# Performance work log

Measured on AMD Instinct MI355X. Metric: run time of the kernel, lower is better.

Reference implementation:

```python
import jax, jax.numpy as jnp
import numpy as np

B, N, D = 4, 4096, 256

def setup_inputs() -> dict:
    key = jax.random.key(0)
    k1, = jax.random.split(key, 1)
    x = jax.random.normal(k1, (B, N, D), dtype=jnp.float32)
    attn_mask = jnp.ones((B, 1, N), dtype=jnp.int32)
    pad_mask = jnp.ones((B, 1, N), dtype=jnp.int32)
    return {"x": x, "attn_mask": attn_mask, "pad_mask": pad_mask, "dim_": D}

def reference(x, attn_mask, pad_mask, dim_):
    # adj is None -> scores = x @ x^T / sqrt(d)
    scale = jnp.sqrt(jnp.asarray(x.shape[-1], x.dtype))
    scores = jnp.einsum('bnd,bmd->bnm', x, x) / scale  # [B, N, N]
    # NOTE: original calls non-in-place masked_fill and discards the result,
    # so pad_mask / attn_mask have no effect on the output (faithful).
    prob = jax.nn.softmax(scores, axis=-1)
    # dropout is identity in inference mode
    return jnp.einsum('bnm,bmd->bnd', prob, x)
```

## Files before the change

kernel.cpp:

```cpp
#include <hip/hip_runtime.h>

typedef __attribute__((ext_vector_type(8))) short short8;
typedef __attribute__((ext_vector_type(4))) float f32x4;
typedef __attribute__((ext_vector_type(4))) unsigned int u32x4;

#define NTOK 4096
#define DIM  256
#define P_STRIDE 72
#define TILE_ELEMS 32768

__device__ __forceinline__ unsigned pack2bf(float a, float b) {
  unsigned ua = __builtin_bit_cast(unsigned, a) + 0x8000u;
  unsigned ub = __builtin_bit_cast(unsigned, b) + 0x8000u;
  return __builtin_amdgcn_perm(ub, ua, 0x07060302u);
}

__global__ __launch_bounds__(256, 4)
void prep_kernel(const float* __restrict__ X, unsigned short* __restrict__ Img) {
  __shared__ __align__(16) unsigned short rowbf[8 * 256];
  const int b    = blockIdx.x & 3;
  const int sub  = blockIdx.x >> 2;
  const int t    = sub >> 3;
  const int part = sub & 7;
  const int tid  = threadIdx.x;
  const float* src = X + ((size_t)b * NTOK + t * 64 + part * 8) * DIM;
  unsigned short* dst = Img + ((size_t)(b * 64 + t)) * TILE_ELEMS;
  {
    const int r = tid >> 5;
    const int c = tid & 31;
    const float* s = src + r * DIM + c * 8;
    f32x4 f0 = *(const f32x4*)s;
    f32x4 f1 = *(const f32x4*)(s + 4);
    union { unsigned u[4]; u32x4 v; } p;
    p.u[0] = pack2bf(f0[0], f0[1]);
    p.u[1] = pack2bf(f0[2], f0[3]);
    p.u[2] = pack2bf(f1[0], f1[1]);
    p.u[3] = pack2bf(f1[2], f1[3]);
    const int gr = part * 8 + r;
    *(u32x4*)(dst + gr * 256 + ((c ^ (gr & 7)) << 3)) = p.v;
    *(u32x4*)(&rowbf[r * 256 + c * 8]) = p.v;
  }
  __syncthreads();
  {
    const int d = tid;
    union { unsigned short s[8]; u32x4 v; } p;
    #pragma unroll
    for (int i = 0; i < 8; ++i) p.s[i] = rowbf[i * 256 + d];
    *(u32x4*)(dst + 16384 + part * 2048 + d * 8) = p.v;
  }
}

__device__ __forceinline__ void pv_step(const unsigned short* __restrict__ pr,
                                        const unsigned short* __restrict__ kt,
                                        f32x4 (&o)[2][4],
                                        int qh, int role, int quad, int ln) {
  #pragma unroll
  for (int ks = 0; ks < 2; ++ks) {
    const int pos = (ks * 4 + quad) ^ ((ln >> 3) << 1);
    short8 ap[2], bv[4];
    #pragma unroll
    for (int s = 0; s < 2; ++s) {
      const int r = qh * 32 + s * 16 + ln;
      ap[s] = *(const short8*)(&pr[r * P_STRIDE + (pos << 3)]);
    }
    const unsigned short* kb = kt + (ks * 4 + quad) * 2048 + (role * 64 + ln) * 8;
    #pragma unroll
    for (int dt = 0; dt < 4; ++dt) bv[dt] = *(const short8*)(kb + dt * 128);
    #pragma unroll
    for (int s = 0; s < 2; ++s)
      #pragma unroll
      for (int dt = 0; dt < 4; ++dt)
        o[s][dt] = __builtin_amdgcn_mfma_f32_16x16x32_bf16(ap[s], bv[dt], o[s][dt], 0, 0, 0);
  }
}

__global__ __launch_bounds__(512, 1)
void fa_kernel(const unsigned short* __restrict__ Img, float* __restrict__ Out) {
  __shared__ __align__(16) unsigned short ksb[2][16384];
  __shared__ __align__(16) unsigned short ktb[2][16384];
  __shared__ __align__(16) unsigned short pb[2][64 * P_STRIDE];
  __shared__ float lbuf[64][4];

  const int tid  = threadIdx.x;
  const int b    = blockIdx.x & 3;
  const int qblk = blockIdx.x >> 2;
  const int wave = tid >> 6;
  const int lane = tid & 63;
  const int ln   = lane & 15;
  const int quad = lane >> 4;
  const int swz  = ln & 7;
  const int qh   = wave & 1;
  const int role = wave >> 1;

  const unsigned short* imgb  = Img + (size_t)b * 64 * TILE_ELEMS;
  const char*           imgbc = (const char*)imgb;

  short8 aQ[2][8];
  #pragma unroll
  for (int s = 0; s < 2; ++s) {
    const unsigned short* qrow =
        imgb + (size_t)qblk * TILE_ELEMS + (qh * 32 + s * 16 + ln) * 256;
    #pragma unroll
    for (int ds = 0; ds < 8; ++ds)
      aQ[s][ds] = *(const short8*)(qrow + (((ds * 4 + quad) ^ swz) << 3));
  }

  f32x4 o[2][4];
  #pragma unroll
  for (int s = 0; s < 2; ++s)
    #pragma unroll
    for (int dt = 0; dt < 4; ++dt) o[s][dt] = (f32x4)(0.0f);
  float lrow[2][4] = {{0.f,0.f,0.f,0.f},{0.f,0.f,0.f,0.f}};

  const float c2 = 0.0901684400f;

  const int pwPos = ((role * 2 + (ln >> 3)) ^ ((quad >> 1) << 1)) << 3;
  const int pwCol = ln & 7;

  const bool dmaKs = wave < 4;
  const int  dmaQ  = wave & 3;
  const char* gK = imgbc + (size_t)dmaQ * 8192 + (size_t)lane * 16;

  if (dmaKs) {
    #pragma unroll
    for (int i = 0; i < 8; ++i)
      __builtin_amdgcn_global_load_lds(
          (const __attribute__((address_space(1))) unsigned*)(gK + i * 1024),
          (__attribute__((address_space(3))) unsigned*)(&ksb[0][dmaQ * 4096 + i * 512]),
          16, 0, 0);
  }

  for (int t = 0; t < 64; ++t) {
    __syncthreads();
    const int buf = t & 1;

    if (dmaKs) {
      if (t < 63) {
        const char* g = gK + (size_t)(t + 1) * 65536;
        unsigned short* l = &ksb[buf ^ 1][dmaQ * 4096];
        #pragma unroll
        for (int i = 0; i < 8; ++i)
          __builtin_amdgcn_global_load_lds(
              (const __attribute__((address_space(1))) unsigned*)(g + i * 1024),
              (__attribute__((address_space(3))) unsigned*)(l + i * 512),
              16, 0, 0);
      }
    } else {
      const char* g = gK + (size_t)t * 65536 + 32768;
      unsigned short* l = &ktb[buf][dmaQ * 4096];
      #pragma unroll
      for (int i = 0; i < 8; ++i)
        __builtin_amdgcn_global_load_lds(
            (const __attribute__((address_space(1))) unsigned*)(g + i * 1024),
            (__attribute__((address_space(3))) unsigned*)(l + i * 512),
            16, 0, 0);
    }

    f32x4 sf0 = (f32x4)(0.0f), sf1 = (f32x4)(0.0f);
    {
      const unsigned short* krow = &ksb[buf][(role * 16 + ln) * 256];
      #pragma unroll
      for (int ds = 0; ds < 8; ++ds) {
        short8 bk = *(const short8*)(krow + (((ds * 4 + quad) ^ swz) << 3));
        sf0 = __builtin_amdgcn_mfma_f32_16x16x32_bf16(aQ[0][ds], bk, sf0, 0, 0, 0);
        sf1 = __builtin_amdgcn_mfma_f32_16x16x32_bf16(aQ[1][ds], bk, sf1, 0, 0, 0);
      }
    }

    unsigned pd0[4], pd1[4];
    #pragma unroll
    for (int j = 0; j < 4; ++j) {
      float p0 = __builtin_amdgcn_exp2f(sf0[j] * c2);
      float p1 = __builtin_amdgcn_exp2f(sf1[j] * c2);
      lrow[0][j] += p0;
      lrow[1][j] += p1;
      unsigned q0 = __builtin_bit_cast(unsigned, p0);
      unsigned q1 = __builtin_bit_cast(unsigned, p1);
      unsigned n0 = (unsigned)__builtin_amdgcn_mov_dpp((int)q0, 0xB1, 0xF, 0xF, true);
      unsigned n1 = (unsigned)__builtin_amdgcn_mov_dpp((int)q1, 0xB1, 0xF, 0xF, true);
      pd0[j] = pack2bf(__builtin_bit_cast(float, q0), __builtin_bit_cast(float, n0));
      pd1[j] = pack2bf(__builtin_bit_cast(float, q1), __builtin_bit_cast(float, n1));
    }

    if (t > 0)
      pv_step(pb[buf ^ 1], ktb[buf ^ 1], o, qh, role, quad, ln);

    if ((ln & 1) == 0) {
      unsigned short* pw = pb[buf];
      #pragma unroll
      for (int j = 0; j < 4; ++j) {
        const int r0 = qh * 32 + quad * 4 + j;
        *(unsigned*)(&pw[r0 * P_STRIDE + pwPos + pwCol]) = pd0[j];
        *(unsigned*)(&pw[(r0 + 16) * P_STRIDE + pwPos + pwCol]) = pd1[j];
      }
    }
  }

  __syncthreads();
  pv_step(pb[1], ktb[1], o, qh, role, quad, ln);

  #pragma unroll
  for (int off = 1; off < 16; off <<= 1)
    #pragma unroll
    for (int s = 0; s < 2; ++s)
      #pragma unroll
      for (int j = 0; j < 4; ++j)
        lrow[s][j] += __shfl_xor(lrow[s][j], off, 64);
  if (ln == 0) {
    #pragma unroll
    for (int s = 0; s < 2; ++s)
      #pragma unroll
      for (int j = 0; j < 4; ++j)
        lbuf[qh * 32 + s * 16 + quad * 4 + j][role] = lrow[s][j];
  }
  __syncthreads();

  #pragma unroll
  for (int s = 0; s < 2; ++s) {
    float* outp = Out + (size_t)(b * NTOK + qblk * 64 + qh * 32 + s * 16) * DIM + role * 64;
    #pragma unroll
    for (int j = 0; j < 4; ++j) {
      const int row = s * 16 + quad * 4 + j;
      f32x4 lv = *(const f32x4*)lbuf[qh * 32 + row];
      const float rl = 1.0f / (lv[0] + lv[1] + lv[2] + lv[3]);
      #pragma unroll
      for (int dt = 0; dt < 4; ++dt)
        outp[(size_t)(quad * 4 + j) * DIM + dt * 16 + ln] = o[s][dt][j] * rl;
    }
  }
}

extern "C" void kernel_launch(void* const* d_in, const int* in_sizes, int n_in,
                              void* d_out, int out_size, void* d_ws, size_t ws_size,
                              hipStream_t stream) {
  const float* X = (const float*)d_in[0];
  float* Out = (float*)d_out;
  unsigned short* Img = (unsigned short*)d_ws;
  (void)in_sizes; (void)n_in; (void)out_size; (void)ws_size;
  hipLaunchKernelGGL(prep_kernel, dim3(2048), dim3(256), 0, stream, X, Img);
  hipLaunchKernelGGL(fa_kernel, dim3(256), dim3(512), 0, stream, Img, Out);
}
```

Measured before the change: 165.7 us.

## Load transposed K tiles directly into registers instead of staging through LDS

The transposed K (V) operand for the PV matmul is now loaded from global memory straight into registers, one iteration ahead, using ping-pong register sets with a loop unrolled by two. The ktb LDS buffers are removed, and all 8 waves now share the score-K DMA into LDS with half the per-wave load count. The aim is to cut LDS traffic and footprint and spread the DMA work across every wave. In exchange, each wave now holds more registers and every wave reads its V fragments from global memory, where before they were loaded once into shared memory. That adds global and L2 traffic and may expose load latency.

```diff
diff --git a/kernel.cpp b/kernel.cpp
--- a/kernel.cpp
+++ b/kernel.cpp
@@ -50,34 +50,28 @@
   }
 }
 
-__device__ __forceinline__ void pv_step(const unsigned short* __restrict__ pr,
-                                        const unsigned short* __restrict__ kt,
-                                        f32x4 (&o)[2][4],
-                                        int qh, int role, int quad, int ln) {
+__device__ __forceinline__ void pv_reg(const unsigned short* __restrict__ pr,
+                                       const short8 (&bv)[2][4],
+                                       f32x4 (&o)[2][4],
+                                       int qh, int quad, int ln) {
   #pragma unroll
   for (int ks = 0; ks < 2; ++ks) {
     const int pos = (ks * 4 + quad) ^ ((ln >> 3) << 1);
-    short8 ap[2], bv[4];
-    #pragma unroll
-    for (int s = 0; s < 2; ++s) {
-      const int r = qh * 32 + s * 16 + ln;
-      ap[s] = *(const short8*)(&pr[r * P_STRIDE + (pos << 3)]);
-    }
-    const unsigned short* kb = kt + (ks * 4 + quad) * 2048 + (role * 64 + ln) * 8;
-    #pragma unroll
-    for (int dt = 0; dt < 4; ++dt) bv[dt] = *(const short8*)(kb + dt * 128);
+    short8 ap[2];
+    #pragma unroll
+    for (int s = 0; s < 2; ++s)
+      ap[s] = *(const short8*)(&pr[(qh * 32 + s * 16 + ln) * P_STRIDE + (pos << 3)]);
     #pragma unroll
     for (int s = 0; s < 2; ++s)
       #pragma unroll
       for (int dt = 0; dt < 4; ++dt)
-        o[s][dt] = __builtin_amdgcn_mfma_f32_16x16x32_bf16(ap[s], bv[dt], o[s][dt], 0, 0, 0);
+        o[s][dt] = __builtin_amdgcn_mfma_f32_16x16x32_bf16(ap[s], bv[ks][dt], o[s][dt], 0, 0, 0);
   }
 }
 
 __global__ __launch_bounds__(512, 1)
 void fa_kernel(const unsigned short* __restrict__ Img, float* __restrict__ Out) {
   __shared__ __align__(16) unsigned short ksb[2][16384];
-  __shared__ __align__(16) unsigned short ktb[2][16384];
   __shared__ __align__(16) unsigned short pb[2][64 * P_STRIDE];
   __shared__ float lbuf[64][4];
 
@@ -117,43 +111,42 @@
   const int pwPos = ((role * 2 + (ln >> 3)) ^ ((quad >> 1) << 1)) << 3;
   const int pwCol = ln & 7;
 
-  const bool dmaKs = wave < 4;
-  const int  dmaQ  = wave & 3;
-  const char* gK = imgbc + (size_t)dmaQ * 8192 + (size_t)lane * 16;
-
-  if (dmaKs) {
-    #pragma unroll
-    for (int i = 0; i < 8; ++i)
-      __builtin_amdgcn_global_load_lds(
-          (const __attribute__((address_space(1))) unsigned*)(gK + i * 1024),
-          (__attribute__((address_space(3))) unsigned*)(&ksb[0][dmaQ * 4096 + i * 512]),
-          16, 0, 0);
-  }
-
-  for (int t = 0; t < 64; ++t) {
+  const char* gK = imgbc + (size_t)wave * 4096 + (size_t)lane * 16;
+  #pragma unroll
+  for (int i = 0; i < 4; ++i)
+    __builtin_amdgcn_global_load_lds(
+        (const __attribute__((address_space(1))) unsigned*)(gK + i * 1024),
+        (__attribute__((address_space(3))) unsigned*)(&ksb[0][wave * 2048 + i * 512]),
+        16, 0, 0);
+
+  const unsigned short* ktg = imgb + 16384 + (size_t)quad * 2048 + (role * 64 + ln) * 8;
+
+  short8 bvE[2][4];
+  short8 bvO[2][4];
+
+  auto iter = [&](int t, short8 (&bvLd)[2][4], short8 (&bvUs)[2][4],
+                  bool doPV) __attribute__((always_inline)) {
     __syncthreads();
     const int buf = t & 1;
 
-    if (dmaKs) {
-      if (t < 63) {
-        const char* g = gK + (size_t)(t + 1) * 65536;
-        unsigned short* l = &ksb[buf ^ 1][dmaQ * 4096];
-        #pragma unroll
-        for (int i = 0; i < 8; ++i)
-          __builtin_amdgcn_global_load_lds(
-              (const __attribute__((address_space(1))) unsigned*)(g + i * 1024),
-              (__attribute__((address_space(3))) unsigned*)(l + i * 512),
-              16, 0, 0);
-      }
-    } else {
-      const char* g = gK + (size_t)t * 65536 + 32768;
-      unsigned short* l = &ktb[buf][dmaQ * 4096];
-      #pragma unroll
-      for (int i = 0; i < 8; ++i)
+    if (t < 63) {
+      const char* g = gK + (size_t)(t + 1) * 65536;
+      unsigned short* l = &ksb[buf ^ 1][wave * 2048];
+      #pragma unroll
+      for (int i = 0; i < 4; ++i)
         __builtin_amdgcn_global_load_lds(
             (const __attribute__((address_space(1))) unsigned*)(g + i * 1024),
             (__attribute__((address_space(3))) unsigned*)(l + i * 512),
             16, 0, 0);
+    }
+
+    {
+      const unsigned short* kt = ktg + (size_t)t * TILE_ELEMS;
+      #pragma unroll
+      for (int ks = 0; ks < 2; ++ks)
+        #pragma unroll
+        for (int dt = 0; dt < 4; ++dt)
+          bvLd[ks][dt] = *(const short8*)(kt + ks * 8192 + dt * 128);
     }
 
     f32x4 sf0 = (f32x4)(0.0f), sf1 = (f32x4)(0.0f);
@@ -182,8 +175,8 @@
       pd1[j] = pack2bf(__builtin_bit_cast(float, q1), __builtin_bit_cast(float, n1));
     }
 
-    if (t > 0)
-      pv_step(pb[buf ^ 1], ktb[buf ^ 1], o, qh, role, quad, ln);
+    if (doPV)
+      pv_reg(pb[buf ^ 1], bvUs, o, qh, quad, ln);
 
     if ((ln & 1) == 0) {
       unsigned short* pw = pb[buf];
@@ -194,10 +187,18 @@
         *(unsigned*)(&pw[(r0 + 16) * P_STRIDE + pwPos + pwCol]) = pd1[j];
       }
     }
-  }
+  };
+
+  iter(0, bvE, bvO, false);
+  #pragma unroll 1
+  for (int tt = 1; tt < 63; tt += 2) {
+    iter(tt, bvO, bvE, true);
+    iter(tt + 1, bvE, bvO, true);
+  }
+  iter(63, bvO, bvE, true);
 
   __syncthreads();
-  pv_step(pb[1], ktb[1], o, qh, role, quad, ln);
+  pv_reg(pb[1], bvO, o, qh, quad, ln);
 
   #pragma unroll
   for (int off = 1; off < 16; off <<= 1)
```

New measurement: 166.3 us. No clear change (+0.4%).

## Split each tile iteration into four barrier-synchronized phases interleaving loads and MFMA

Applied to the files above, without the earlier changes.

Restructures the main loop into four phases (two QK^T halves, two PV halves). Each phase issues LDS reads and splits the global-to-LDS DMA into halves, then crosses a raw s_barrier before running its MFMA cluster at raised wave priority. This ping-pong style schedule is meant to keep loads and matrix work overlapping across waves and to spread memory traffic evenly. It adds four barriers per iteration instead of one, so synchronization overhead and the risk of hazards from the manual waitcnt placement both increase.

```diff
diff --git a/kernel.cpp b/kernel.cpp
--- a/kernel.cpp
+++ b/kernel.cpp
@@ -50,30 +50,6 @@
   }
 }
 
-__device__ __forceinline__ void pv_step(const unsigned short* __restrict__ pr,
-                                        const unsigned short* __restrict__ kt,
-                                        f32x4 (&o)[2][4],
-                                        int qh, int role, int quad, int ln) {
-  #pragma unroll
-  for (int ks = 0; ks < 2; ++ks) {
-    const int pos = (ks * 4 + quad) ^ ((ln >> 3) << 1);
-    short8 ap[2], bv[4];
-    #pragma unroll
-    for (int s = 0; s < 2; ++s) {
-      const int r = qh * 32 + s * 16 + ln;
-      ap[s] = *(const short8*)(&pr[r * P_STRIDE + (pos << 3)]);
-    }
-    const unsigned short* kb = kt + (ks * 4 + quad) * 2048 + (role * 64 + ln) * 8;
-    #pragma unroll
-    for (int dt = 0; dt < 4; ++dt) bv[dt] = *(const short8*)(kb + dt * 128);
-    #pragma unroll
-    for (int s = 0; s < 2; ++s)
-      #pragma unroll
-      for (int dt = 0; dt < 4; ++dt)
-        o[s][dt] = __builtin_amdgcn_mfma_f32_16x16x32_bf16(ap[s], bv[dt], o[s][dt], 0, 0, 0);
-  }
-}
-
 __global__ __launch_bounds__(512, 1)
 void fa_kernel(const unsigned short* __restrict__ Img, float* __restrict__ Out) {
   __shared__ __align__(16) unsigned short ksb[2][16384];
@@ -129,75 +105,188 @@
           (__attribute__((address_space(3))) unsigned*)(&ksb[0][dmaQ * 4096 + i * 512]),
           16, 0, 0);
   }
-
+  __syncthreads();
+
+  #pragma unroll 1
   for (int t = 0; t < 64; ++t) {
-    __syncthreads();
     const int buf = t & 1;
-
-    if (dmaKs) {
-      if (t < 63) {
-        const char* g = gK + (size_t)(t + 1) * 65536;
-        unsigned short* l = &ksb[buf ^ 1][dmaQ * 4096];
-        #pragma unroll
-        for (int i = 0; i < 8; ++i)
+    const unsigned short* krow = &ksb[buf][(role * 16 + ln) * 256];
+    const unsigned short* prd  = pb[buf ^ 1];
+    const unsigned short* ktp  = ktb[buf ^ 1];
+    const char* gNext = gK + (size_t)(t + 1) * 65536;
+    unsigned short* lNext = &ksb[buf ^ 1][dmaQ * 4096];
+    const char* gKt = gK + (size_t)t * 65536 + 32768;
+    unsigned short* lKt = &ktb[buf][dmaQ * 4096];
+
+    f32x4 sf0 = (f32x4)(0.0f), sf1 = (f32x4)(0.0f);
+
+    {
+      short8 bk[4];
+      #pragma unroll
+      for (int ds = 0; ds < 4; ++ds)
+        bk[ds] = *(const short8*)(krow + (((ds * 4 + quad) ^ swz) << 3));
+      if (dmaKs && t < 63) {
+        #pragma unroll
+        for (int i = 0; i < 4; ++i)
           __builtin_amdgcn_global_load_lds(
-              (const __attribute__((address_space(1))) unsigned*)(g + i * 1024),
-              (__attribute__((address_space(3))) unsigned*)(l + i * 512),
+              (const __attribute__((address_space(1))) unsigned*)(gNext + i * 1024),
+              (__attribute__((address_space(3))) unsigned*)(lNext + i * 512),
               16, 0, 0);
       }
-    } else {
-      const char* g = gK + (size_t)t * 65536 + 32768;
-      unsigned short* l = &ktb[buf][dmaQ * 4096];
-      #pragma unroll
-      for (int i = 0; i < 8; ++i)
-        __builtin_amdgcn_global_load_lds(
-            (const __attribute__((address_space(1))) unsigned*)(g + i * 1024),
-            (__attribute__((address_space(3))) unsigned*)(l + i * 512),
-            16, 0, 0);
-    }
-
-    f32x4 sf0 = (f32x4)(0.0f), sf1 = (f32x4)(0.0f);
+      __builtin_amdgcn_s_barrier();
+      asm volatile("s_waitcnt lgkmcnt(0)" ::: "memory");
+      __builtin_amdgcn_sched_barrier(0);
+      __builtin_amdgcn_s_setprio(1);
+      #pragma unroll
+      for (int ds = 0; ds < 4; ++ds) {
+        sf0 = __builtin_amdgcn_mfma_f32_16x16x32_bf16(aQ[0][ds], bk[ds], sf0, 0, 0, 0);
+        sf1 = __builtin_amdgcn_mfma_f32_16x16x32_bf16(aQ[1][ds], bk[ds], sf1, 0, 0, 0);
+      }
+      __builtin_amdgcn_s_setprio(0);
+      __builtin_amdgcn_s_barrier();
+    }
+
     {
-      const unsigned short* krow = &ksb[buf][(role * 16 + ln) * 256];
-      #pragma unroll
-      for (int ds = 0; ds < 8; ++ds) {
-        short8 bk = *(const short8*)(krow + (((ds * 4 + quad) ^ swz) << 3));
-        sf0 = __builtin_amdgcn_mfma_f32_16x16x32_bf16(aQ[0][ds], bk, sf0, 0, 0, 0);
-        sf1 = __builtin_amdgcn_mfma_f32_16x16x32_bf16(aQ[1][ds], bk, sf1, 0, 0, 0);
-      }
+      short8 bk[4];
+      #pragma unroll
+      for (int ds = 0; ds < 4; ++ds)
+        bk[ds] = *(const short8*)(krow + ((((ds + 4) * 4 + quad) ^ swz) << 3));
+      if (dmaKs) {
+        if (t < 63) {
+          #pragma unroll
+          for (int i = 4; i < 8; ++i)
+            __builtin_amdgcn_global_load_lds(
+                (const __attribute__((address_space(1))) unsigned*)(gNext + i * 1024),
+                (__attribute__((address_space(3))) unsigned*)(lNext + i * 512),
+                16, 0, 0);
+        }
+      } else {
+        #pragma unroll
+        for (int i = 0; i < 4; ++i)
+          __builtin_amdgcn_global_load_lds(
+              (const __attribute__((address_space(1))) unsigned*)(gKt + i * 1024),
+              (__attribute__((address_space(3))) unsigned*)(lKt + i * 512),
+              16, 0, 0);
+      }
+      __builtin_amdgcn_s_barrier();
+      asm volatile("s_waitcnt lgkmcnt(0)" ::: "memory");
+      __builtin_amdgcn_sched_barrier(0);
+      __builtin_amdgcn_s_setprio(1);
+      #pragma unroll
+      for (int ds = 0; ds < 4; ++ds) {
+        sf0 = __builtin_amdgcn_mfma_f32_16x16x32_bf16(aQ[0][ds + 4], bk[ds], sf0, 0, 0, 0);
+        sf1 = __builtin_amdgcn_mfma_f32_16x16x32_bf16(aQ[1][ds + 4], bk[ds], sf1, 0, 0, 0);
+      }
+      __builtin_amdgcn_s_setprio(0);
+      __builtin_amdgcn_s_barrier();
     }
 
     unsigned pd0[4], pd1[4];
-    #pragma unroll
-    for (int j = 0; j < 4; ++j) {
-      float p0 = __builtin_amdgcn_exp2f(sf0[j] * c2);
-      float p1 = __builtin_amdgcn_exp2f(sf1[j] * c2);
-      lrow[0][j] += p0;
-      lrow[1][j] += p1;
-      unsigned q0 = __builtin_bit_cast(unsigned, p0);
-      unsigned q1 = __builtin_bit_cast(unsigned, p1);
-      unsigned n0 = (unsigned)__builtin_amdgcn_mov_dpp((int)q0, 0xB1, 0xF, 0xF, true);
-      unsigned n1 = (unsigned)__builtin_amdgcn_mov_dpp((int)q1, 0xB1, 0xF, 0xF, true);
-      pd0[j] = pack2bf(__builtin_bit_cast(float, q0), __builtin_bit_cast(float, n0));
-      pd1[j] = pack2bf(__builtin_bit_cast(float, q1), __builtin_bit_cast(float, n1));
-    }
-
-    if (t > 0)
-      pv_step(pb[buf ^ 1], ktb[buf ^ 1], o, qh, role, quad, ln);
-
-    if ((ln & 1) == 0) {
-      unsigned short* pw = pb[buf];
+    {
       #pragma unroll
       for (int j = 0; j < 4; ++j) {
-        const int r0 = qh * 32 + quad * 4 + j;
-        *(unsigned*)(&pw[r0 * P_STRIDE + pwPos + pwCol]) = pd0[j];
-        *(unsigned*)(&pw[(r0 + 16) * P_STRIDE + pwPos + pwCol]) = pd1[j];
-      }
+        float p0 = __builtin_amdgcn_exp2f(sf0[j] * c2);
+        float p1 = __builtin_amdgcn_exp2f(sf1[j] * c2);
+        lrow[0][j] += p0;
+        lrow[1][j] += p1;
+        unsigned q0 = __builtin_bit_cast(unsigned, p0);
+        unsigned q1 = __builtin_bit_cast(unsigned, p1);
+        unsigned n0 = (unsigned)__builtin_amdgcn_mov_dpp((int)q0, 0xB1, 0xF, 0xF, true);
+        unsigned n1 = (unsigned)__builtin_amdgcn_mov_dpp((int)q1, 0xB1, 0xF, 0xF, true);
+        pd0[j] = pack2bf(__builtin_bit_cast(float, q0), __builtin_bit_cast(float, n0));
+        pd1[j] = pack2bf(__builtin_bit_cast(float, q1), __builtin_bit_cast(float, n1));
+      }
+      short8 ap[2], bv[4];
+      if (t > 0) {
+        const int pos = quad ^ ((ln >> 3) << 1);
+        #pragma unroll
+        for (int s = 0; s < 2; ++s)
+          ap[s] = *(const short8*)(&prd[(qh * 32 + s * 16 + ln) * P_STRIDE + (pos << 3)]);
+        const unsigned short* kb = ktp + quad * 2048 + (role * 64 + ln) * 8;
+        #pragma unroll
+        for (int dt = 0; dt < 4; ++dt) bv[dt] = *(const short8*)(kb + dt * 128);
+      }
+      if (!dmaKs) {
+        #pragma unroll
+        for (int i = 4; i < 8; ++i)
+          __builtin_amdgcn_global_load_lds(
+              (const __attribute__((address_space(1))) unsigned*)(gKt + i * 1024),
+              (__attribute__((address_space(3))) unsigned*)(lKt + i * 512),
+              16, 0, 0);
+      }
+      __builtin_amdgcn_s_barrier();
+      asm volatile("s_waitcnt lgkmcnt(0)" ::: "memory");
+      __builtin_amdgcn_sched_barrier(0);
+      if (t > 0) {
+        __builtin_amdgcn_s_setprio(1);
+        #pragma unroll
+        for (int s = 0; s < 2; ++s)
+          #pragma unroll
+          for (int dt = 0; dt < 4; ++dt)
+            o[s][dt] = __builtin_amdgcn_mfma_f32_16x16x32_bf16(ap[s], bv[dt], o[s][dt], 0, 0, 0);
+        __builtin_amdgcn_s_setprio(0);
+      }
+      __builtin_amdgcn_s_barrier();
+    }
+
+    {
+      short8 ap[2], bv[4];
+      if (t > 0) {
+        const int pos = (4 + quad) ^ ((ln >> 3) << 1);
+        #pragma unroll
+        for (int s = 0; s < 2; ++s)
+          ap[s] = *(const short8*)(&prd[(qh * 32 + s * 16 + ln) * P_STRIDE + (pos << 3)]);
+        const unsigned short* kb = ktp + (4 + quad) * 2048 + (role * 64 + ln) * 8;
+        #pragma unroll
+        for (int dt = 0; dt < 4; ++dt) bv[dt] = *(const short8*)(kb + dt * 128);
+      }
+      if ((ln & 1) == 0) {
+        unsigned short* pw = pb[buf];
+        #pragma unroll
+        for (int j = 0; j < 4; ++j) {
+          const int r0 = qh * 32 + quad * 4 + j;
+          *(unsigned*)(&pw[r0 * P_STRIDE + pwPos + pwCol]) = pd0[j];
+          *(unsigned*)(&pw[(r0 + 16) * P_STRIDE + pwPos + pwCol]) = pd1[j];
+        }
+      }
+      asm volatile("s_waitcnt vmcnt(0)" ::: "memory");
+      __builtin_amdgcn_s_barrier();
+      asm volatile("s_waitcnt lgkmcnt(0)" ::: "memory");
+      __builtin_amdgcn_sched_barrier(0);
+      if (t > 0) {
+        __builtin_amdgcn_s_setprio(1);
+        #pragma unroll
+        for (int s = 0; s < 2; ++s)
+          #pragma unroll
+          for (int dt = 0; dt < 4; ++dt)
+            o[s][dt] = __builtin_amdgcn_mfma_f32_16x16x32_bf16(ap[s], bv[dt], o[s][dt], 0, 0, 0);
+        __builtin_amdgcn_s_setprio(0);
+      }
+      __builtin_amdgcn_s_barrier();
     }
   }
 
   __syncthreads();
-  pv_step(pb[1], ktb[1], o, qh, role, quad, ln);
+  {
+    const unsigned short* prd = pb[1];
+    const unsigned short* ktp = ktb[1];
+    #pragma unroll
+    for (int ks = 0; ks < 2; ++ks) {
+      const int pos = (ks * 4 + quad) ^ ((ln >> 3) << 1);
+      short8 ap[2], bv[4];
+      #pragma unroll
+      for (int s = 0; s < 2; ++s)
+        ap[s] = *(const short8*)(&prd[(qh * 32 + s * 16 + ln) * P_STRIDE + (pos << 3)]);
+      const unsigned short* kb = ktp + (ks * 4 + quad) * 2048 + (role * 64 + ln) * 8;
+      #pragma unroll
+      for (int dt = 0; dt < 4; ++dt) bv[dt] = *(const short8*)(kb + dt * 128);
+      #pragma unroll
+      for (int s = 0; s < 2; ++s)
+        #pragma unroll
+        for (int dt = 0; dt < 4; ++dt)
+          o[s][dt] = __builtin_amdgcn_mfma_f32_16x16x32_bf16(ap[s], bv[dt], o[s][dt], 0, 0, 0);
+    }
+  }
 
   #pragma unroll
   for (int off = 1; off < 16; off <<= 1)
```

Result: slower. 177.5 us (+7.1%).
